# Optimization experiments

Measured on AMD Instinct MI355X. Metric: run time of the kernel, lower is better.

## Reference

```python
import jax, jax.numpy as jnp
import numpy as np

B, C, H, W = 8, 256, 64, 64
HEADS, R, TOPK_FRAC = 8, 4, 0.25
DIM = C // HEADS
SCALE = DIM ** -0.5


def setup_inputs() -> dict:
    key = jax.random.key(0)
    ks = jax.random.split(key, 8)
    s = 0.05
    return {
        "x": jax.random.normal(ks[0], (B, C, H, W), jnp.float32),
        "w_q": jax.random.normal(ks[1], (C, C), jnp.float32) * s,
        "w_k": jax.random.normal(ks[2], (C, C), jnp.float32) * s,
        "w_v": jax.random.normal(ks[3], (C, C), jnp.float32) * s,
        "w_ck": jax.random.normal(ks[4], (C, R, R), jnp.float32) * s,  # depthwise kxk
        "w_cv": jax.random.normal(ks[5], (C, R, R), jnp.float32) * s,
        "w_out": jax.random.normal(ks[6], (C, C), jnp.float32) * s,
        "b_out": jax.random.normal(ks[7], (C,), jnp.float32) * s,
    }


def _conv1x1(x, w):
    # x: [B,C,H,W], w: [O,C]
    return jnp.einsum('bchw,oc->bohw', x, w)


def _depthwise_pool(x, w):
    # depthwise conv, kernel=stride=R -> non-overlapping blocks
    b, c, h, wd = x.shape
    blocks = x.reshape(b, c, h // R, R, wd // R, R)
    return jnp.einsum('bcirjs,crs->bcij', blocks, w)


def reference(x, w_q, w_k, w_v, w_ck, w_cv, w_out, b_out):
    N = H * W
    q = _conv1x1(x, w_q)
    k = _conv1x1(x, w_k)
    v = _conv1x1(x, w_v)
    k_s = _depthwise_pool(k, w_ck)   # [B,C,H/R,W/R]
    v_s = _depthwise_pool(v, w_cv)
    n = k_s.shape[2] * k_s.shape[3]

    BH = B * HEADS
    q = q.reshape(B, HEADS, DIM, N).reshape(BH, DIM, N)
    k = k_s.reshape(B, HEADS, DIM, n).reshape(BH, DIM, n)
    v = v_s.reshape(B, HEADS, DIM, n).reshape(BH, DIM, n)

    # stage 1: full queries vs compressed keys
    attn = jax.nn.softmax(jnp.einsum('bdi,bdj->bij', q, k) * SCALE, axis=-1)
    token_score = attn.sum(axis=1)                     # [BH, n]
    top_k = max(1, int(n * TOPK_FRAC))
    _, idx = jax.lax.top_k(token_score, top_k)         # [BH, top_k]

    idx_exp = jnp.broadcast_to(idx[:, None, :], (BH, DIM, top_k))
    k_top = jnp.take_along_axis(k, idx_exp, axis=2)    # [BH, DIM, top_k]
    v_top = jnp.take_along_axis(v, idx_exp, axis=2)

    # stage 2: attend only to selected compressed tokens
    attn_full = jax.nn.softmax(jnp.einsum('bdi,bdj->bij', q, k_top) * SCALE, axis=-1)
    out = jnp.einsum('bij,bdj->bdi', attn_full, v_top)  # [BH, DIM, N]
    out = out.reshape(B, HEADS, DIM, N).reshape(B, C, H, W)
    return _conv1x1(out, w_out) + b_out[None, :, None, None]
```

## Files before the change

### kernel.cpp

```cpp
#include <hip/hip_runtime.h>

#define Bq 8
#define Cq 256
#define Hq 64
#define Wq 64
#define Nq 4096
#define HEADSq 8
#define DIMq 32
#define NCq 256
#define TOPKq 64
#define BHq 64
#define SCALEq 0.17677669529663687f

typedef short bf16x8 __attribute__((ext_vector_type(8)));
typedef float f32x16 __attribute__((ext_vector_type(16)));

__device__ __forceinline__ uint32_t f2bf_hi(float f) {
  uint32_t u = __float_as_uint(f);
  return (u + 0x7FFFu + ((u >> 16) & 1u)) >> 16;
}

__device__ __forceinline__ void split8(const float* v, uint4& hv, uint4& lv) {
  uint32_t h[8], l[8];
#pragma unroll
  for (int j = 0; j < 8; ++j) {
    uint32_t hb = f2bf_hi(v[j]);
    float rest = v[j] - __uint_as_float(hb << 16);
    h[j] = hb;
    l[j] = __float_as_uint(rest) >> 16;
  }
  hv = make_uint4(h[0] | (h[1] << 16), h[2] | (h[3] << 16),
                  h[4] | (h[5] << 16), h[6] | (h[7] << 16));
  lv = make_uint4(l[0] | (l[1] << 16), l[2] | (l[3] << 16),
                  l[4] | (l[5] << 16), l[6] | (l[7] << 16));
}


__global__ __launch_bounds__(256) void prep_w(
    const float* __restrict__ wq, const float* __restrict__ wk,
    const float* __restrict__ wv, const float* __restrict__ wo,
    char* __restrict__ wt) {
  const int oblk = blockIdx.x, s = blockIdx.y, mat = blockIdx.z;
  const float* w = mat == 0 ? wq : mat == 1 ? wk : mat == 2 ? wv : wo;
  const int t = threadIdx.x;
  const int o = t & 63, g = t >> 6;
  float v[8];
  const float* src = w + (size_t)(oblk * 64 + o) * Cq + s * 32 + g * 8;
#pragma unroll
  for (int j = 0; j < 8; ++j) v[j] = src[j];
  uint4 hv, lv;
  split8(v, hv, lv);
  size_t base = ((size_t)((mat * 4 + oblk) * 8 + s)) * 8192;
  int off = ((o >> 5) * 2 + (g >> 1)) * 1024 + ((o & 31) + 32 * (g & 1)) * 16;
  *(uint4*)(wt + base + off) = hv;
  *(uint4*)(wt + base + 4096 + off) = lv;
}

__global__ __launch_bounds__(256) void qkv_mfma(
    const float* __restrict__ x, const char* __restrict__ wt,
    float* __restrict__ q, float* __restrict__ kf, float* __restrict__ vf) {
  const int b = blockIdx.z, oblk = blockIdx.y, nblk = blockIdx.x;
  const int o0 = oblk * 64, n0 = nblk * 64;
  const int t = threadIdx.x, l = t & 63, wid = t >> 6;
  const int ob = wid >> 1, nbw = wid & 1;
  __shared__ __align__(16) short wimg[3][2][2048];
  __shared__ __align__(16) short ximg[2][2048];
  __shared__ __align__(16) float xf[32][64];
  f32x16 acc[3];
#pragma unroll
  for (int m = 0; m < 3; ++m)
#pragma unroll
    for (int i = 0; i < 16; ++i) acc[m][i] = 0.f;

  for (int s = 0; s < 8; ++s) {
    __syncthreads();
#pragma unroll
    for (int i = 0; i < 6; ++i) {
      const int m = i >> 1;
      const int off = t + (i & 1) * 256;
      ((uint4*)&wimg[m][0][0])[off] =
          ((const uint4*)(wt + ((size_t)((m * 4 + oblk) * 8 + s)) * 8192))[off];
    }
    {
      const float* xb = x + ((size_t)(b * Cq + s * 32)) * Nq + n0;
#pragma unroll
      for (int i = 0; i < 2; ++i) {
        int e = t + i * 256;
        int cl = e >> 4, n4 = (e & 15) * 4;
        *(float4*)&xf[cl][n4] = *(const float4*)&xb[(size_t)cl * Nq + n4];
      }
    }
    __syncthreads();
    {
      int n = t & 63, g = t >> 6;
      float v[8];
#pragma unroll
      for (int j = 0; j < 8; ++j) v[j] = xf[g * 8 + j][n];
      uint4 hv, lv;
      split8(v, hv, lv);
      int off = ((n >> 5) * 2 + (g >> 1)) * 1024 + ((n & 31) + 32 * (g & 1)) * 16;
      *(uint4*)((char*)&ximg[0][0] + off) = hv;
      *(uint4*)((char*)&ximg[1][0] + off) = lv;
    }
    __syncthreads();
    bf16x8 bh[2], bl[2];
#pragma unroll
    for (int kh = 0; kh < 2; ++kh) {
      int off = (nbw * 2 + kh) * 1024 + l * 16;
      bh[kh] = *(const bf16x8*)((const char*)&ximg[0][0] + off);
      bl[kh] = *(const bf16x8*)((const char*)&ximg[1][0] + off);
    }
#pragma unroll
    for (int m = 0; m < 3; ++m) {
#pragma unroll
      for (int kh = 0; kh < 2; ++kh) {
        int off = (ob * 2 + kh) * 1024 + l * 16;
        bf16x8 ah = *(const bf16x8*)((const char*)&wimg[m][0][0] + off);
        bf16x8 al = *(const bf16x8*)((const char*)&wimg[m][1][0] + off);
        acc[m] = __builtin_amdgcn_mfma_f32_32x32x16_bf16(ah, bh[kh], acc[m], 0, 0, 0);
        acc[m] = __builtin_amdgcn_mfma_f32_32x32x16_bf16(ah, bl[kh], acc[m], 0, 0, 0);
        acc[m] = __builtin_amdgcn_mfma_f32_32x32x16_bf16(al, bh[kh], acc[m], 0, 0, 0);
      }
    }
  }
#pragma unroll
  for (int m = 0; m < 3; ++m) {
    float* dst = (m == 0 ? q : m == 1 ? kf : vf) + (size_t)b * Cq * Nq;
#pragma unroll
    for (int r = 0; r < 16; ++r) {
      int orow = o0 + ob * 32 + (r & 3) + 8 * (r >> 2) + 4 * (l >> 5);
      dst[(size_t)orow * Nq + n0 + nbw * 32 + (l & 31)] = acc[m][r];
    }
  }
}

__global__ __launch_bounds__(256) void pool_kv(
    const float* __restrict__ kf, const float* __restrict__ vf,
    const float* __restrict__ wck, const float* __restrict__ wcv,
    float* __restrict__ ks, float* __restrict__ vs) {
  int bc = blockIdx.x;
  int b = bc / Cq, c = bc % Cq;
  int t = threadIdx.x;
  int i = t >> 4, j = t & 15;
  const float* kp = kf + ((size_t)b * Cq + c) * Nq;
  const float* vp = vf + ((size_t)b * Cq + c) * Nq;
  __shared__ float wk_s[16], wv_s[16];
  if (t < 16) { wk_s[t] = wck[c * 16 + t]; wv_s[t] = wcv[c * 16 + t]; }
  __syncthreads();
  float ak = 0.f, av = 0.f;
#pragma unroll
  for (int r = 0; r < 4; ++r)
#pragma unroll
    for (int s = 0; s < 4; ++s) {
      int n = (i * 4 + r) * Wq + j * 4 + s;
      float wkv = wk_s[r * 4 + s], wvv = wv_s[r * 4 + s];
      ak += kp[n] * wkv;
      av += vp[n] * wvv;
    }
  ks[((size_t)b * Cq + c) * NCq + t] = ak;
  vs[((size_t)b * Cq + c) * NCq + t] = av;
}

__global__ __launch_bounds__(256, 2) void stage1_mfma(
    const float* __restrict__ q, const float* __restrict__ ks,
    float* __restrict__ part) {
  const int bh = blockIdx.y, b = bh >> 3, h = bh & 7;
  const int row0 = blockIdx.x * 512;
  const int t = threadIdx.x, l = t & 63, wid = t >> 6;
  __shared__ __align__(16) short kimg[2][4][2048];
  __shared__ __align__(16) short qimg[2][2][2048];
  __shared__ __align__(16) float xf[32][128];
  __shared__ float sc[4][256];

  const float* qb = q + ((size_t)b * Cq + h * DIMq) * Nq;
  const float* kb = ks + ((size_t)b * Cq + h * DIMq) * NCq;

#pragma unroll
  for (int half = 0; half < 2; ++half) {
    __syncthreads();
#pragma unroll
    for (int i = 0; i < 4; ++i) {
      int row = (t >> 5) + i * 8, c4 = (t & 31) * 4;
      *(float4*)&xf[row][c4] =
          *(const float4*)&kb[(size_t)row * NCq + half * 128 + c4];
    }
    __syncthreads();
#pragma unroll
    for (int i = 0; i < 2; ++i) {
      int e = t + i * 256;
      int n = e & 127, g = e >> 7;
      float v[8];
#pragma unroll
      for (int j = 0; j < 8; ++j) v[j] = xf[g * 8 + j][n];
      uint4 hv, lv;
      split8(v, hv, lv);
      int img = half * 2 + (n >> 6), row = n & 63;
      int off = ((row >> 5) * 2 + (g >> 1)) * 1024 +
                ((row & 31) + 32 * (g & 1)) * 16;
      *(uint4*)((char*)&kimg[0][img][0] + off) = hv;
      *(uint4*)((char*)&kimg[1][img][0] + off) = lv;
    }
  }

  float scoreacc[8];
#pragma unroll
  for (int g = 0; g < 8; ++g) scoreacc[g] = 0.f;

  for (int step = 0; step < 4; ++step) {
    const int r0 = row0 + step * 128;
    __syncthreads();
#pragma unroll
    for (int i = 0; i < 4; ++i) {
      int row = (t >> 5) + i * 8, c4 = (t & 31) * 4;
      *(float4*)&xf[row][c4] = *(const float4*)&qb[(size_t)row * Nq + r0 + c4];
    }
    __syncthreads();
#pragma unroll
    for (int i = 0; i < 2; ++i) {
      int e = t + i * 256;
      int n = e & 127, g = e >> 7;
      float v[8];
#pragma unroll
      for (int j = 0; j < 8; ++j) v[j] = xf[g * 8 + j][n];
      uint4 hv, lv;
      split8(v, hv, lv);
      int img = n >> 6, row = n & 63;
      int off = ((row >> 5) * 2 + (g >> 1)) * 1024 +
                ((row & 31) + 32 * (g & 1)) * 16;
      *(uint4*)((char*)&qimg[0][img][0] + off) = hv;
      *(uint4*)((char*)&qimg[1][img][0] + off) = lv;
    }
    __syncthreads();
    bf16x8 ah[2], al[2];
#pragma unroll
    for (int kh = 0; kh < 2; ++kh) {
      int off = ((wid & 1) * 2 + kh) * 1024 + l * 16;
      ah[kh] = *(const bf16x8*)((const char*)&qimg[0][wid >> 1][0] + off);
      al[kh] = *(const bf16x8*)((const char*)&qimg[1][wid >> 1][0] + off);
    }
    f32x16 acc[8];
#pragma unroll
    for (int g = 0; g < 8; ++g)
#pragma unroll
      for (int r = 0; r < 16; ++r) acc[g][r] = 0.f;
#pragma unroll
    for (int img = 0; img < 4; ++img)
#pragma unroll
      for (int nb = 0; nb < 2; ++nb) {
        const int g = img * 2 + nb;
#pragma unroll
        for (int kh = 0; kh < 2; ++kh) {
          int off = (nb * 2 + kh) * 1024 + l * 16;
          bf16x8 bh = *(const bf16x8*)((const char*)&kimg[0][img][0] + off);
          bf16x8 bl = *(const bf16x8*)((const char*)&kimg[1][img][0] + off);
          acc[g] = __builtin_amdgcn_mfma_f32_32x32x16_bf16(ah[kh], bh, acc[g], 0, 0, 0);
          acc[g] = __builtin_amdgcn_mfma_f32_32x32x16_bf16(ah[kh], bl, acc[g], 0, 0, 0);
          acc[g] = __builtin_amdgcn_mfma_f32_32x32x16_bf16(al[kh], bh, acc[g], 0, 0, 0);
        }
      }
    float mx[16], sm[16];
#pragma unroll
    for (int r = 0; r < 16; ++r) {
      float m = acc[0][r];
#pragma unroll
      for (int g = 1; g < 8; ++g) m = fmaxf(m, acc[g][r]);
      mx[r] = m;
    }
#pragma unroll
    for (int off = 1; off < 32; off <<= 1)
#pragma unroll
      for (int r = 0; r < 16; ++r) mx[r] = fmaxf(mx[r], __shfl_xor(mx[r], off));
#pragma unroll
    for (int r = 0; r < 16; ++r) sm[r] = 0.f;
#pragma unroll
    for (int g = 0; g < 8; ++g)
#pragma unroll
      for (int r = 0; r < 16; ++r) {
        float e = __expf((acc[g][r] - mx[r]) * SCALEq);
        acc[g][r] = e;
        sm[r] += e;
      }
#pragma unroll
    for (int off = 1; off < 32; off <<= 1)
#pragma unroll
      for (int r = 0; r < 16; ++r) sm[r] += __shfl_xor(sm[r], off);
#pragma unroll
    for (int r = 0; r < 16; ++r) sm[r] = 1.0f / sm[r];
#pragma unroll
    for (int g = 0; g < 8; ++g) {
      float tp = 0.f;
#pragma unroll
      for (int r = 0; r < 16; ++r) tp += acc[g][r] * sm[r];
      tp += __shfl_xor(tp, 32);
      scoreacc[g] += tp;
    }
  }
  if (l < 32) {
#pragma unroll
    for (int g = 0; g < 8; ++g) sc[wid][g * 32 + l] = scoreacc[g];
  }
  __syncthreads();
  {
    float v = sc[0][t] + sc[1][t] + sc[2][t] + sc[3][t];
    part[((size_t)bh * 8 + blockIdx.x) * NCq + t] = v;
  }
}

__global__ __launch_bounds__(256) void reduce_scores(
    const float* __restrict__ part, float* __restrict__ score) {
  int bh = blockIdx.x, t = threadIdx.x;
  float s = 0.f;
#pragma unroll
  for (int c = 0; c < 8; ++c) s += part[((size_t)bh * 8 + c) * NCq + t];
  score[bh * NCq + t] = s;
}

__global__ __launch_bounds__(256) void topk_sel(
    const float* __restrict__ score, int* __restrict__ idx) {
  int bh = blockIdx.x, t = threadIdx.x;
  __shared__ float s[NCq];
  s[t] = score[bh * NCq + t];
  __syncthreads();
  float st = s[t];
  int rank = 0;
  for (int j = 0; j < NCq; ++j) {
    float sj = s[j];
    rank += (sj > st) || (sj == st && j < t);
  }
  if (rank < TOPKq) idx[bh * TOPKq + rank] = t;
}

__global__ __launch_bounds__(256, 2) void stage2_mfma(
    const float* __restrict__ q, const float* __restrict__ ks,
    const float* __restrict__ vs, const int* __restrict__ idx,
    char* __restrict__ at) {
  const int bh = blockIdx.y, b = bh >> 3, h = bh & 7;
  const int n0 = blockIdx.x * 128;
  const int t = threadIdx.x, l = t & 63, wid = t >> 6;
  __shared__ __align__(16) short kimg[2][2048];
  __shared__ __align__(16) short vimg[2][2][1024];
  __shared__ __align__(16) short qimg[2][2][2048];
  __shared__ float pbuf[128][66];
  __shared__ int ibs[64];

  const float* qb = q + ((size_t)b * Cq + h * DIMq) * Nq;
  const float* ksb = ks + ((size_t)b * Cq + h * DIMq) * NCq;
  const float* vsb = vs + ((size_t)b * Cq + h * DIMq) * NCq;
  if (t < 64) ibs[t] = idx[bh * TOPKq + t];
  __syncthreads();

  {
    int tok = t & 63, dg = t >> 6;
    int ti = ibs[tok];
    float v[8];
#pragma unroll
    for (int j = 0; j < 8; ++j) v[j] = ksb[(size_t)(dg * 8 + j) * NCq + ti];
    uint4 hv, lv;
    split8(v, hv, lv);
    int off = ((tok >> 5) * 2 + (dg >> 1)) * 1024 + ((tok & 31) + 32 * (dg & 1)) * 16;
    *(uint4*)((char*)&kimg[0][0] + off) = hv;
    *(uint4*)((char*)&kimg[1][0] + off) = lv;
  }
  {
    int d = l & 31, tko = l >> 5, img = (t >> 6) >> 1, kreg = (t >> 6) & 1;
    float v[8];
#pragma unroll
    for (int j = 0; j < 8; ++j) {
      int tok = img * 32 + kreg * 16 + tko * 8 + j;
      v[j] = vsb[(size_t)d * NCq + ibs[tok]];
    }
    uint4 hv, lv;
    split8(v, hv, lv);
    int off = kreg * 1024 + (d + 32 * tko) * 16;
    *(uint4*)((char*)&vimg[0][img][0] + off) = hv;
    *(uint4*)((char*)&vimg[1][img][0] + off) = lv;
  }
#pragma unroll
  for (int qi = 0; qi < 2; ++qi) {
    int qr = t & 63, dg = t >> 6;
    float v[8];
#pragma unroll
    for (int j = 0; j < 8; ++j)
      v[j] = qb[(size_t)(dg * 8 + j) * Nq + n0 + qi * 64 + qr];
    uint4 hv, lv;
    split8(v, hv, lv);
    int off = ((qr >> 5) * 2 + (dg >> 1)) * 1024 + ((qr & 31) + 32 * (dg & 1)) * 16;
    *(uint4*)((char*)&qimg[0][qi][0] + off) = hv;
    *(uint4*)((char*)&qimg[1][qi][0] + off) = lv;
  }
  __syncthreads();

  f32x16 pacc[2];
#pragma unroll
  for (int g = 0; g < 2; ++g)
#pragma unroll
    for (int r = 0; r < 16; ++r) pacc[g][r] = 0.f;
  {
    bf16x8 ah[2], al[2];
#pragma unroll
    for (int kd = 0; kd < 2; ++kd) {
      int off = ((wid & 1) * 2 + kd) * 1024 + l * 16;
      ah[kd] = *(const bf16x8*)((const char*)&qimg[0][wid >> 1][0] + off);
      al[kd] = *(const bf16x8*)((const char*)&qimg[1][wid >> 1][0] + off);
    }
#pragma unroll
    for (int g = 0; g < 2; ++g)
#pragma unroll
      for (int kd = 0; kd < 2; ++kd) {
        int off = (g * 2 + kd) * 1024 + l * 16;
        bf16x8 bh = *(const bf16x8*)((const char*)&kimg[0][0] + off);
        bf16x8 bl = *(const bf16x8*)((const char*)&kimg[1][0] + off);
        pacc[g] = __builtin_amdgcn_mfma_f32_32x32x16_bf16(ah[kd], bh, pacc[g], 0, 0, 0);
        pacc[g] = __builtin_amdgcn_mfma_f32_32x32x16_bf16(ah[kd], bl, pacc[g], 0, 0, 0);
        pacc[g] = __builtin_amdgcn_mfma_f32_32x32x16_bf16(al[kd], bh, pacc[g], 0, 0, 0);
      }
  }
  {
    float mx[16], sm[16];
#pragma unroll
    for (int r = 0; r < 16; ++r) mx[r] = fmaxf(pacc[0][r], pacc[1][r]);
#pragma unroll
    for (int off = 1; off < 32; off <<= 1)
#pragma unroll
      for (int r = 0; r < 16; ++r) mx[r] = fmaxf(mx[r], __shfl_xor(mx[r], off));
#pragma unroll
    for (int r = 0; r < 16; ++r) {
      float e0 = __expf((pacc[0][r] - mx[r]) * SCALEq);
      float e1 = __expf((pacc[1][r] - mx[r]) * SCALEq);
      pacc[0][r] = e0; pacc[1][r] = e1;
      sm[r] = e0 + e1;
    }
#pragma unroll
    for (int off = 1; off < 32; off <<= 1)
#pragma unroll
      for (int r = 0; r < 16; ++r) sm[r] += __shfl_xor(sm[r], off);
#pragma unroll
    for (int r = 0; r < 16; ++r) sm[r] = 1.0f / sm[r];
#pragma unroll
    for (int g = 0; g < 2; ++g)
#pragma unroll
      for (int r = 0; r < 16; ++r) {
        int qrow = wid * 32 + (r & 3) + 8 * (r >> 2) + 4 * (l >> 5);
        pbuf[qrow][g * 32 + (l & 31)] = pacc[g][r] * sm[r];
      }
  }
  __syncthreads();
  f32x16 oacc;
#pragma unroll
  for (int r = 0; r < 16; ++r) oacc[r] = 0.f;
#pragma unroll
  for (int ks4 = 0; ks4 < 4; ++ks4) {
    const float* pa = &pbuf[wid * 32 + (l & 31)][ks4 * 16 + (l >> 5) * 8];
    float v[8];
#pragma unroll
    for (int j = 0; j < 8; ++j) v[j] = pa[j];
    uint4 hv, lv;
    split8(v, hv, lv);
    bf16x8 pah = *(const bf16x8*)&hv, pal = *(const bf16x8*)&lv;
    int off = (ks4 & 1) * 1024 + l * 16;
    bf16x8 bh = *(const bf16x8*)((const char*)&vimg[0][ks4 >> 1][0] + off);
    bf16x8 bl = *(const bf16x8*)((const char*)&vimg[1][ks4 >> 1][0] + off);
    oacc = __builtin_amdgcn_mfma_f32_32x32x16_bf16(pah, bh, oacc, 0, 0, 0);
    oacc = __builtin_amdgcn_mfma_f32_32x32x16_bf16(pah, bl, oacc, 0, 0, 0);
    oacc = __builtin_amdgcn_mfma_f32_32x32x16_bf16(pal, bh, oacc, 0, 0, 0);
  }
#pragma unroll
  for (int r = 0; r < 16; ++r) {
    int qrow = wid * 32 + (r & 3) + 8 * (r >> 2) + 4 * (l >> 5);
    pbuf[qrow][l & 31] = oacc[r];
  }
  __syncthreads();
#pragma unroll
  for (int i = 0; i < 2; ++i) {
    int slot = t + i * 256;
    int row = slot >> 2, dg = slot & 3;
    float v[8];
#pragma unroll
    for (int j = 0; j < 8; ++j) v[j] = pbuf[row][dg * 8 + j];
    uint4 hv, lv;
    split8(v, hv, lv);
    int nb = blockIdx.x * 2 + (row >> 6), nloc = row & 63;
    size_t base = ((size_t)((b * 64 + nb) * 8 + h)) * 8192;
    int off = ((nloc >> 5) * 2 + (dg >> 1)) * 1024 +
              ((nloc & 31) + 32 * (dg & 1)) * 16;
    *(uint4*)(at + base + off) = hv;
    *(uint4*)(at + base + 4096 + off) = lv;
  }
}

__global__ __launch_bounds__(256) void out_mfma(
    const char* __restrict__ at, const char* __restrict__ wt,
    const float* __restrict__ bo, float* __restrict__ y) {
  const int b = blockIdx.z, oblk = blockIdx.y, nblk = blockIdx.x;
  const int o0 = oblk * 64, n0 = nblk * 64;
  const int t = threadIdx.x, l = t & 63, wid = t >> 6;
  const int ob = wid >> 1, nbw = wid & 1;
  __shared__ __align__(16) short wimg[2][2048];
  __shared__ __align__(16) short ximg[2][2048];
  __shared__ float bs[64];
  if (t < 64) bs[t] = bo[o0 + t];
  f32x16 acc;
#pragma unroll
  for (int i = 0; i < 16; ++i) acc[i] = 0.f;

  for (int s = 0; s < 8; ++s) {
    __syncthreads();
    {
      const uint4* srcw = (const uint4*)(wt + ((size_t)((12 + oblk) * 8 + s)) * 8192);
      const uint4* srcx = (const uint4*)(at + ((size_t)((b * 64 + nblk) * 8 + s)) * 8192);
#pragma unroll
      for (int i = 0; i < 2; ++i) {
        ((uint4*)&wimg[0][0])[t + i * 256] = srcw[t + i * 256];
        ((uint4*)&ximg[0][0])[t + i * 256] = srcx[t + i * 256];
      }
    }
    __syncthreads();
#pragma unroll
    for (int kh = 0; kh < 2; ++kh) {
      int offa = (ob * 2 + kh) * 1024 + l * 16;
      int offb = (nbw * 2 + kh) * 1024 + l * 16;
      bf16x8 ah = *(const bf16x8*)((const char*)&wimg[0][0] + offa);
      bf16x8 al = *(const bf16x8*)((const char*)&wimg[1][0] + offa);
      bf16x8 bh = *(const bf16x8*)((const char*)&ximg[0][0] + offb);
      bf16x8 bl = *(const bf16x8*)((const char*)&ximg[1][0] + offb);
      acc = __builtin_amdgcn_mfma_f32_32x32x16_bf16(ah, bh, acc, 0, 0, 0);
      acc = __builtin_amdgcn_mfma_f32_32x32x16_bf16(ah, bl, acc, 0, 0, 0);
      acc = __builtin_amdgcn_mfma_f32_32x32x16_bf16(al, bh, acc, 0, 0, 0);
    }
  }
#pragma unroll
  for (int r = 0; r < 16; ++r) {
    int ol = ob * 32 + (r & 3) + 8 * (r >> 2) + 4 * (l >> 5);
    y[((size_t)(b * Cq + o0 + ol)) * Nq + n0 + nbw * 32 + (l & 31)] = acc[r] + bs[ol];
  }
}

extern "C" void kernel_launch(void* const* d_in, const int* in_sizes, int n_in,
                              void* d_out, int out_size, void* d_ws, size_t ws_size,
                              hipStream_t stream) {
  const float* x   = (const float*)d_in[0];
  const float* wq  = (const float*)d_in[1];
  const float* wk  = (const float*)d_in[2];
  const float* wv  = (const float*)d_in[3];
  const float* wck = (const float*)d_in[4];
  const float* wcv = (const float*)d_in[5];
  const float* wo  = (const float*)d_in[6];
  const float* bo  = (const float*)d_in[7];
  float* out = (float*)d_out;

  float* ws = (float*)d_ws;
  const size_t SZ_FULL = (size_t)Bq * Cq * Nq;
  const size_t SZ_CMP  = (size_t)Bq * Cq * NCq;
  float* q     = ws;
  float* kf    = q  + SZ_FULL;
  float* vf    = kf + SZ_FULL;
  float* ksc   = vf + SZ_FULL;
  float* vsc   = ksc + SZ_CMP;
  float* part  = vsc + SZ_CMP;
  float* score = part + (size_t)BHq * 8 * NCq;
  int*   idx   = (int*)(score + (size_t)BHq * NCq);
  char*  wt    = (char*)(idx + (size_t)BHq * TOPKq);
  char*  at    = (char*)kf;

  prep_w<<<dim3(4, 8, 4), 256, 0, stream>>>(wq, wk, wv, wo, wt);
  qkv_mfma<<<dim3(64, 4, 8), 256, 0, stream>>>(x, wt, q, kf, vf);
  pool_kv<<<dim3(Bq * Cq), 256, 0, stream>>>(kf, vf, wck, wcv, ksc, vsc);
  stage1_mfma<<<dim3(8, BHq), 256, 0, stream>>>(q, ksc, part);
  reduce_scores<<<dim3(BHq), 256, 0, stream>>>(part, score);
  topk_sel<<<dim3(BHq), 256, 0, stream>>>(score, idx);
  stage2_mfma<<<dim3(32, BHq), 256, 0, stream>>>(q, ksc, vsc, idx, at);
  out_mfma<<<dim3(64, 4, 8), 256, 0, stream>>>(at, wt, bo, out);
}
```

Measured before the change: 185.3 us.

## Fuse QKV projection with depthwise pooling and emit pre-split bf16 Q images

The QKV projection now writes Q directly as pre-split bf16 hi/lo MFMA operand images and applies the depthwise 4x4 pooling in its epilogue, so full-resolution K and V are never written to memory. A separate prep_x kernel pre-splits x into bf16 images once, and a prep_w32 kernel prepares 32-row weight tiles. Stage1 and stage2 load Q operands straight from global memory instead of converting fp32 Q in shared memory each time. This removes the large fp32 K/V round trip, the separate pool kernel and repeated Q conversion, at the cost of extra prep launches and an extra x-image write and read.

```diff
diff --git a/kernel.cpp b/kernel.cpp
--- a/kernel.cpp
+++ b/kernel.cpp
@@ -56,138 +56,185 @@
   *(uint4*)(wt + base + 4096 + off) = lv;
 }
 
-__global__ __launch_bounds__(256) void qkv_mfma(
-    const float* __restrict__ x, const char* __restrict__ wt,
-    float* __restrict__ q, float* __restrict__ kf, float* __restrict__ vf) {
-  const int b = blockIdx.z, oblk = blockIdx.y, nblk = blockIdx.x;
-  const int o0 = oblk * 64, n0 = nblk * 64;
+__global__ __launch_bounds__(128) void prep_w32(
+    const float* __restrict__ wq, const float* __restrict__ wk,
+    const float* __restrict__ wv, char* __restrict__ wt32) {
+  const int oblk = blockIdx.x, s = blockIdx.y, mat = blockIdx.z;
+  const float* w = mat == 0 ? wq : mat == 1 ? wk : wv;
+  const int t = threadIdx.x;
+  const int o = t & 31, g = t >> 5;
+  float v[8];
+  const float* src = w + (size_t)(oblk * 32 + o) * Cq + s * 32 + g * 8;
+#pragma unroll
+  for (int j = 0; j < 8; ++j) v[j] = src[j];
+  uint4 hv, lv;
+  split8(v, hv, lv);
+  size_t base = ((size_t)((mat * 8 + oblk) * 8 + s)) * 4096;
+  int off = (g >> 1) * 1024 + (o + 32 * (g & 1)) * 16;
+  *(uint4*)(wt32 + base + off) = hv;
+  *(uint4*)(wt32 + base + 2048 + off) = lv;
+}
+
+__global__ __launch_bounds__(256) void prep_x(
+    const float* __restrict__ x, char* __restrict__ xt) {
+  const int n64 = blockIdx.x, s = blockIdx.y, b = blockIdx.z;
+  const int t = threadIdx.x;
+  __shared__ float xf[32][64];
+  const float* xb = x + ((size_t)(b * Cq + s * 32)) * Nq + n64 * 64;
+#pragma unroll
+  for (int ii = 0; ii < 2; ++ii) {
+    int e = t + ii * 256;
+    int cl = e >> 4, n4 = (e & 15) * 4;
+    *(float4*)&xf[cl][n4] = *(const float4*)&xb[(size_t)cl * Nq + n4];
+  }
+  __syncthreads();
+  int n = t & 63, g = t >> 6;
+  float v[8];
+#pragma unroll
+  for (int j = 0; j < 8; ++j) v[j] = xf[g * 8 + j][n];
+  uint4 hv, lv;
+  split8(v, hv, lv);
+  char* dst = xt + ((size_t)((b * 8 + s) * 128 + n64 * 2 + (n >> 5))) * 4096;
+  int off = (g >> 1) * 1024 + ((n & 31) + 32 * (g & 1)) * 16;
+  *(uint4*)(dst + off) = hv;
+  *(uint4*)(dst + 2048 + off) = lv;
+}
+
+__global__ __launch_bounds__(256) void qkv_fused(
+    const char* __restrict__ wt32, const char* __restrict__ xt,
+    const float* __restrict__ wck, const float* __restrict__ wcv,
+    char* __restrict__ qimg, float* __restrict__ ksc, float* __restrict__ vsc) {
+  const int i = blockIdx.x, oblk = blockIdx.y, b = blockIdx.z;
   const int t = threadIdx.x, l = t & 63, wid = t >> 6;
-  const int ob = wid >> 1, nbw = wid & 1;
-  __shared__ __align__(16) short wimg[3][2][2048];
-  __shared__ __align__(16) short ximg[2][2048];
-  __shared__ __align__(16) float xf[32][64];
-  f32x16 acc[3];
+  __shared__ __align__(16) short wimg[3][2][1024];
+  __shared__ float qf[32][256];
+  __shared__ float pp[4][2][32][16];
+  __shared__ float wpool[2][32][16];
+
+  for (int u = t; u < 1024; u += 256) {
+    int m = u >> 9, c = (u >> 4) & 31, e = u & 15;
+    wpool[m][c][e] = (m ? wcv : wck)[(oblk * 32 + c) * 16 + e];
+  }
+
+  f32x16 acc[3][2];
 #pragma unroll
   for (int m = 0; m < 3; ++m)
 #pragma unroll
-    for (int i = 0; i < 16; ++i) acc[m][i] = 0.f;
+    for (int nt = 0; nt < 2; ++nt)
+#pragma unroll
+      for (int r = 0; r < 16; ++r) acc[m][nt][r] = 0.f;
 
   for (int s = 0; s < 8; ++s) {
     __syncthreads();
 #pragma unroll
-    for (int i = 0; i < 6; ++i) {
-      const int m = i >> 1;
-      const int off = t + (i & 1) * 256;
-      ((uint4*)&wimg[m][0][0])[off] =
-          ((const uint4*)(wt + ((size_t)((m * 4 + oblk) * 8 + s)) * 8192))[off];
-    }
-    {
-      const float* xb = x + ((size_t)(b * Cq + s * 32)) * Nq + n0;
-#pragma unroll
-      for (int i = 0; i < 2; ++i) {
-        int e = t + i * 256;
-        int cl = e >> 4, n4 = (e & 15) * 4;
-        *(float4*)&xf[cl][n4] = *(const float4*)&xb[(size_t)cl * Nq + n4];
-      }
+    for (int u = 0; u < 3; ++u) {
+      int e = t + u * 256;
+      int m = e >> 8, r = e & 255;
+      ((uint4*)&wimg[m][0][0])[r] =
+          ((const uint4*)(wt32 + ((size_t)((m * 8 + oblk) * 8 + s)) * 4096))[r];
     }
     __syncthreads();
-    {
-      int n = t & 63, g = t >> 6;
+    bf16x8 xh[2][2], xl[2][2];
+#pragma unroll
+    for (int nt = 0; nt < 2; ++nt) {
+      const char* xb = xt + ((size_t)((b * 8 + s) * 128 + i * 8 + wid * 2 + nt)) * 4096;
+#pragma unroll
+      for (int kh = 0; kh < 2; ++kh) {
+        int off = kh * 1024 + l * 16;
+        xh[nt][kh] = *(const bf16x8*)(xb + off);
+        xl[nt][kh] = *(const bf16x8*)(xb + 2048 + off);
+      }
+    }
+#pragma unroll
+    for (int m = 0; m < 3; ++m)
+#pragma unroll
+      for (int kh = 0; kh < 2; ++kh) {
+        int off = kh * 1024 + l * 16;
+        bf16x8 ah = *(const bf16x8*)((const char*)&wimg[m][0][0] + off);
+        bf16x8 al = *(const bf16x8*)((const char*)&wimg[m][1][0] + off);
+#pragma unroll
+        for (int nt = 0; nt < 2; ++nt) {
+          acc[m][nt] = __builtin_amdgcn_mfma_f32_32x32x16_bf16(ah, xh[nt][kh], acc[m][nt], 0, 0, 0);
+          acc[m][nt] = __builtin_amdgcn_mfma_f32_32x32x16_bf16(ah, xl[nt][kh], acc[m][nt], 0, 0, 0);
+          acc[m][nt] = __builtin_amdgcn_mfma_f32_32x32x16_bf16(al, xh[nt][kh], acc[m][nt], 0, 0, 0);
+        }
+      }
+  }
+
+#pragma unroll
+  for (int nt = 0; nt < 2; ++nt)
+#pragma unroll
+    for (int r = 0; r < 16; ++r) {
+      int c_l = (r & 3) + 8 * (r >> 2) + 4 * (l >> 5);
+      qf[c_l][wid * 64 + nt * 32 + (l & 31)] = acc[0][nt][r];
+    }
+#pragma unroll
+  for (int m = 1; m <= 2; ++m)
+#pragma unroll
+    for (int nt = 0; nt < 2; ++nt)
+#pragma unroll
+      for (int r = 0; r < 16; ++r) {
+        int c_l = (r & 3) + 8 * (r >> 2) + 4 * (l >> 5);
+        float sv = acc[m][nt][r] * wpool[m - 1][c_l][wid * 4 + (l & 3)];
+        float t0 = sv + __shfl_xor(sv, 1);
+        float s4 = t0 + __shfl_xor(t0, 2);
+        if ((l & 3) == 0)
+          pp[wid][m - 1][c_l][nt * 8 + ((l & 31) >> 2)] = s4;
+      }
+  __syncthreads();
+  const int bh = b * 8 + oblk;
+  {
+    int row = t & 63, dg = t >> 6;
+#pragma unroll
+    for (int rb = 0; rb < 4; ++rb) {
       float v[8];
 #pragma unroll
-      for (int j = 0; j < 8; ++j) v[j] = xf[g * 8 + j][n];
+      for (int j = 0; j < 8; ++j) v[j] = qf[dg * 8 + j][rb * 64 + row];
       uint4 hv, lv;
       split8(v, hv, lv);
-      int off = ((n >> 5) * 2 + (g >> 1)) * 1024 + ((n & 31) + 32 * (g & 1)) * 16;
-      *(uint4*)((char*)&ximg[0][0] + off) = hv;
-      *(uint4*)((char*)&ximg[1][0] + off) = lv;
-    }
-    __syncthreads();
-    bf16x8 bh[2], bl[2];
-#pragma unroll
-    for (int kh = 0; kh < 2; ++kh) {
-      int off = (nbw * 2 + kh) * 1024 + l * 16;
-      bh[kh] = *(const bf16x8*)((const char*)&ximg[0][0] + off);
-      bl[kh] = *(const bf16x8*)((const char*)&ximg[1][0] + off);
-    }
-#pragma unroll
-    for (int m = 0; m < 3; ++m) {
-#pragma unroll
-      for (int kh = 0; kh < 2; ++kh) {
-        int off = (ob * 2 + kh) * 1024 + l * 16;
-        bf16x8 ah = *(const bf16x8*)((const char*)&wimg[m][0][0] + off);
-        bf16x8 al = *(const bf16x8*)((const char*)&wimg[m][1][0] + off);
-        acc[m] = __builtin_amdgcn_mfma_f32_32x32x16_bf16(ah, bh[kh], acc[m], 0, 0, 0);
-        acc[m] = __builtin_amdgcn_mfma_f32_32x32x16_bf16(ah, bl[kh], acc[m], 0, 0, 0);
-        acc[m] = __builtin_amdgcn_mfma_f32_32x32x16_bf16(al, bh[kh], acc[m], 0, 0, 0);
-      }
-    }
-  }
-#pragma unroll
-  for (int m = 0; m < 3; ++m) {
-    float* dst = (m == 0 ? q : m == 1 ? kf : vf) + (size_t)b * Cq * Nq;
-#pragma unroll
-    for (int r = 0; r < 16; ++r) {
-      int orow = o0 + ob * 32 + (r & 3) + 8 * (r >> 2) + 4 * (l >> 5);
-      dst[(size_t)orow * Nq + n0 + nbw * 32 + (l & 31)] = acc[m][r];
-    }
-  }
-}
-
-__global__ __launch_bounds__(256) void pool_kv(
-    const float* __restrict__ kf, const float* __restrict__ vf,
-    const float* __restrict__ wck, const float* __restrict__ wcv,
-    float* __restrict__ ks, float* __restrict__ vs) {
-  int bc = blockIdx.x;
-  int b = bc / Cq, c = bc % Cq;
-  int t = threadIdx.x;
-  int i = t >> 4, j = t & 15;
-  const float* kp = kf + ((size_t)b * Cq + c) * Nq;
-  const float* vp = vf + ((size_t)b * Cq + c) * Nq;
-  __shared__ float wk_s[16], wv_s[16];
-  if (t < 16) { wk_s[t] = wck[c * 16 + t]; wv_s[t] = wcv[c * 16 + t]; }
-  __syncthreads();
-  float ak = 0.f, av = 0.f;
-#pragma unroll
-  for (int r = 0; r < 4; ++r)
-#pragma unroll
-    for (int s = 0; s < 4; ++s) {
-      int n = (i * 4 + r) * Wq + j * 4 + s;
-      float wkv = wk_s[r * 4 + s], wvv = wv_s[r * 4 + s];
-      ak += kp[n] * wkv;
-      av += vp[n] * wvv;
-    }
-  ks[((size_t)b * Cq + c) * NCq + t] = ak;
-  vs[((size_t)b * Cq + c) * NCq + t] = av;
+      char* qb = qimg + ((size_t)(bh * 64 + i * 4 + rb)) * 8192;
+      int off = ((row >> 5) * 2 + (dg >> 1)) * 1024 + ((row & 31) + 32 * (dg & 1)) * 16;
+      *(uint4*)(qb + off) = hv;
+      *(uint4*)(qb + 4096 + off) = lv;
+    }
+  }
+  {
+    int c = t >> 3, jj = t & 7;
+#pragma unroll
+    for (int m = 0; m < 2; ++m)
+#pragma unroll
+      for (int rep = 0; rep < 2; ++rep) {
+        int j = jj + rep * 8;
+        float v = pp[0][m][c][j] + pp[1][m][c][j] + pp[2][m][c][j] + pp[3][m][c][j];
+        float* dst = m ? vsc : ksc;
+        dst[((size_t)b * Cq + oblk * 32 + c) * NCq + i * 16 + j] = v;
+      }
+  }
 }
 
 __global__ __launch_bounds__(256, 2) void stage1_mfma(
-    const float* __restrict__ q, const float* __restrict__ ks,
+    const char* __restrict__ qim, const float* __restrict__ ks,
     float* __restrict__ part) {
   const int bh = blockIdx.y, b = bh >> 3, h = bh & 7;
-  const int row0 = blockIdx.x * 512;
   const int t = threadIdx.x, l = t & 63, wid = t >> 6;
   __shared__ __align__(16) short kimg[2][4][2048];
-  __shared__ __align__(16) short qimg[2][2][2048];
   __shared__ __align__(16) float xf[32][128];
   __shared__ float sc[4][256];
 
-  const float* qb = q + ((size_t)b * Cq + h * DIMq) * Nq;
   const float* kb = ks + ((size_t)b * Cq + h * DIMq) * NCq;
-
 #pragma unroll
   for (int half = 0; half < 2; ++half) {
     __syncthreads();
 #pragma unroll
-    for (int i = 0; i < 4; ++i) {
-      int row = (t >> 5) + i * 8, c4 = (t & 31) * 4;
+    for (int ii = 0; ii < 4; ++ii) {
+      int row = (t >> 5) + ii * 8, c4 = (t & 31) * 4;
       *(float4*)&xf[row][c4] =
           *(const float4*)&kb[(size_t)row * NCq + half * 128 + c4];
     }
     __syncthreads();
 #pragma unroll
-    for (int i = 0; i < 2; ++i) {
-      int e = t + i * 256;
+    for (int ii = 0; ii < 2; ++ii) {
+      int e = t + ii * 256;
       int n = e & 127, g = e >> 7;
       float v[8];
 #pragma unroll
@@ -201,42 +248,21 @@
       *(uint4*)((char*)&kimg[1][img][0] + off) = lv;
     }
   }
+  __syncthreads();
 
   float scoreacc[8];
 #pragma unroll
   for (int g = 0; g < 8; ++g) scoreacc[g] = 0.f;
 
   for (int step = 0; step < 4; ++step) {
-    const int r0 = row0 + step * 128;
-    __syncthreads();
-#pragma unroll
-    for (int i = 0; i < 4; ++i) {
-      int row = (t >> 5) + i * 8, c4 = (t & 31) * 4;
-      *(float4*)&xf[row][c4] = *(const float4*)&qb[(size_t)row * Nq + r0 + c4];
-    }
-    __syncthreads();
-#pragma unroll
-    for (int i = 0; i < 2; ++i) {
-      int e = t + i * 256;
-      int n = e & 127, g = e >> 7;
-      float v[8];
-#pragma unroll
-      for (int j = 0; j < 8; ++j) v[j] = xf[g * 8 + j][n];
-      uint4 hv, lv;
-      split8(v, hv, lv);
-      int img = n >> 6, row = n & 63;
-      int off = ((row >> 5) * 2 + (g >> 1)) * 1024 +
-                ((row & 31) + 32 * (g & 1)) * 16;
-      *(uint4*)((char*)&qimg[0][img][0] + off) = hv;
-      *(uint4*)((char*)&qimg[1][img][0] + off) = lv;
-    }
-    __syncthreads();
+    const int rowblk = blockIdx.x * 8 + step * 2 + (wid >> 1);
+    const char* qb = qim + ((size_t)(bh * 64 + rowblk)) * 8192;
     bf16x8 ah[2], al[2];
 #pragma unroll
     for (int kh = 0; kh < 2; ++kh) {
       int off = ((wid & 1) * 2 + kh) * 1024 + l * 16;
-      ah[kh] = *(const bf16x8*)((const char*)&qimg[0][wid >> 1][0] + off);
-      al[kh] = *(const bf16x8*)((const char*)&qimg[1][wid >> 1][0] + off);
+      ah[kh] = *(const bf16x8*)(qb + off);
+      al[kh] = *(const bf16x8*)(qb + 4096 + off);
     }
     f32x16 acc[8];
 #pragma unroll
@@ -331,19 +357,16 @@
 }
 
 __global__ __launch_bounds__(256, 2) void stage2_mfma(
-    const float* __restrict__ q, const float* __restrict__ ks,
+    const char* __restrict__ qim, const float* __restrict__ ks,
     const float* __restrict__ vs, const int* __restrict__ idx,
     char* __restrict__ at) {
   const int bh = blockIdx.y, b = bh >> 3, h = bh & 7;
-  const int n0 = blockIdx.x * 128;
   const int t = threadIdx.x, l = t & 63, wid = t >> 6;
   __shared__ __align__(16) short kimg[2][2048];
   __shared__ __align__(16) short vimg[2][2][1024];
-  __shared__ __align__(16) short qimg[2][2][2048];
   __shared__ float pbuf[128][66];
   __shared__ int ibs[64];
 
-  const float* qb = q + ((size_t)b * Cq + h * DIMq) * Nq;
   const float* ksb = ks + ((size_t)b * Cq + h * DIMq) * NCq;
   const float* vsb = vs + ((size_t)b * Cq + h * DIMq) * NCq;
   if (t < 64) ibs[t] = idx[bh * TOPKq + t];
@@ -375,19 +398,6 @@
     *(uint4*)((char*)&vimg[0][img][0] + off) = hv;
     *(uint4*)((char*)&vimg[1][img][0] + off) = lv;
   }
-#pragma unroll
-  for (int qi = 0; qi < 2; ++qi) {
-    int qr = t & 63, dg = t >> 6;
-    float v[8];
-#pragma unroll
-    for (int j = 0; j < 8; ++j)
-      v[j] = qb[(size_t)(dg * 8 + j) * Nq + n0 + qi * 64 + qr];
-    uint4 hv, lv;
-    split8(v, hv, lv);
-    int off = ((qr >> 5) * 2 + (dg >> 1)) * 1024 + ((qr & 31) + 32 * (dg & 1)) * 16;
-    *(uint4*)((char*)&qimg[0][qi][0] + off) = hv;
-    *(uint4*)((char*)&qimg[1][qi][0] + off) = lv;
-  }
   __syncthreads();
 
   f32x16 pacc[2];
@@ -396,12 +406,13 @@
 #pragma unroll
     for (int r = 0; r < 16; ++r) pacc[g][r] = 0.f;
   {
+    const char* qb = qim + ((size_t)(bh * 64 + blockIdx.x * 2 + (wid >> 1))) * 8192;
     bf16x8 ah[2], al[2];
 #pragma unroll
     for (int kd = 0; kd < 2; ++kd) {
       int off = ((wid & 1) * 2 + kd) * 1024 + l * 16;
-      ah[kd] = *(const bf16x8*)((const char*)&qimg[0][wid >> 1][0] + off);
-      al[kd] = *(const bf16x8*)((const char*)&qimg[1][wid >> 1][0] + off);
+      ah[kd] = *(const bf16x8*)(qb + off);
+      al[kd] = *(const bf16x8*)(qb + 4096 + off);
     }
 #pragma unroll
     for (int g = 0; g < 2; ++g)
@@ -471,8 +482,8 @@
   }
   __syncthreads();
 #pragma unroll
-  for (int i = 0; i < 2; ++i) {
-    int slot = t + i * 256;
+  for (int ii = 0; ii < 2; ++ii) {
+    int slot = t + ii * 256;
     int row = slot >> 2, dg = slot & 3;
     float v[8];
 #pragma unroll
@@ -548,26 +559,25 @@
   const float* bo  = (const float*)d_in[7];
   float* out = (float*)d_out;
 
-  float* ws = (float*)d_ws;
-  const size_t SZ_FULL = (size_t)Bq * Cq * Nq;
-  const size_t SZ_CMP  = (size_t)Bq * Cq * NCq;
-  float* q     = ws;
-  float* kf    = q  + SZ_FULL;
-  float* vf    = kf + SZ_FULL;
-  float* ksc   = vf + SZ_FULL;
-  float* vsc   = ksc + SZ_CMP;
-  float* part  = vsc + SZ_CMP;
+  char* wsb = (char*)d_ws;
+  char*  qimg = wsb;
+  char*  xt   = wsb + (size_t)33554432;
+  char*  at   = xt;
+  char*  wt   = wsb + (size_t)67108864;
+  char*  wt32 = wsb + (size_t)68157440;
+  float* ksc  = (float*)(wsb + (size_t)68943872);
+  float* vsc  = ksc + (size_t)Bq * Cq * NCq;
+  float* part = vsc + (size_t)Bq * Cq * NCq;
   float* score = part + (size_t)BHq * 8 * NCq;
-  int*   idx   = (int*)(score + (size_t)BHq * NCq);
-  char*  wt    = (char*)(idx + (size_t)BHq * TOPKq);
-  char*  at    = (char*)kf;
+  int*   idx  = (int*)(score + (size_t)BHq * NCq);
 
   prep_w<<<dim3(4, 8, 4), 256, 0, stream>>>(wq, wk, wv, wo, wt);
-  qkv_mfma<<<dim3(64, 4, 8), 256, 0, stream>>>(x, wt, q, kf, vf);
-  pool_kv<<<dim3(Bq * Cq), 256, 0, stream>>>(kf, vf, wck, wcv, ksc, vsc);
-  stage1_mfma<<<dim3(8, BHq), 256, 0, stream>>>(q, ksc, part);
+  prep_w32<<<dim3(8, 8, 3), 128, 0, stream>>>(wq, wk, wv, wt32);
+  prep_x<<<dim3(64, 8, 8), 256, 0, stream>>>(x, xt);
+  qkv_fused<<<dim3(16, 8, 8), 256, 0, stream>>>(wt32, xt, wck, wcv, qimg, ksc, vsc);
+  stage1_mfma<<<dim3(8, BHq), 256, 0, stream>>>(qimg, ksc, part);
   reduce_scores<<<dim3(BHq), 256, 0, stream>>>(part, score);
   topk_sel<<<dim3(BHq), 256, 0, stream>>>(score, idx);
-  stage2_mfma<<<dim3(32, BHq), 256, 0, stream>>>(q, ksc, vsc, idx, at);
+  stage2_mfma<<<dim3(32, BHq), 256, 0, stream>>>(qimg, ksc, vsc, idx, at);
   out_mfma<<<dim3(64, 4, 8), 256, 0, stream>>>(at, wt, bo, out);
 }
```

Result: slower. 200.3 us (+8.1%).
